# Performance work log

Hardware: AMD Instinct MI355X
Metric: run time of the kernel (lower is better)

Reference implementation:

```python
import jax, jax.numpy as jnp
import numpy as np

B, N, XD = 64, 512, 32  # batch, n_points, x_dims (feature columns); last 2 cols are t, y


def setup_inputs() -> dict:
    key = jax.random.key(0)
    xtys = jax.random.normal(key, (B, N, XD + 2), dtype=jnp.float32)
    return {"xtys": xtys}


def _linear_dml(xtys):
    b, n, D = xtys.shape
    d = D - 2
    xs = xtys[..., :d]          # (b, n, d) covariates
    ts = xtys[..., d]           # (b, n)   treatment
    ys = xtys[..., d + 1]       # (b, n)   outcome

    # Growing-prefix least squares via cumulative sufficient statistics.
    # For prefix i (rows 0..i): min-norm lstsq solution w = pinv(X^T X) X^T v == pinv(X) v,
    # matching torch.linalg.lstsq (gelsy/gelsd) semantics including rank-deficient prefixes.
    G = jnp.cumsum(jnp.einsum('bnd,bne->bnde', xs, xs), axis=1)      # (b,n,d,d) Gram
    Xty = jnp.cumsum(xs * ys[..., None], axis=1)                     # (b,n,d)
    Xtt = jnp.cumsum(xs * ts[..., None], axis=1)                     # (b,n,d)
    Sty = jnp.cumsum(ts * ys, axis=1)                                # (b,n)
    Stt = jnp.cumsum(ts * ts, axis=1)                                # (b,n)

    Ginv = jnp.linalg.pinv(G)                                        # batched pinv, (b,n,d,d)
    wy = jnp.einsum('bnde,bne->bnd', Ginv, Xty)
    wt = jnp.einsum('bnde,bne->bnd', Ginv, Xtt)

    # ate_i = <t_res, y_res> / <t_res, t_res> over prefix, expanded via the stats above.
    num = (Sty
           - jnp.einsum('bnd,bnd->bn', wt, Xty)
           - jnp.einsum('bnd,bnd->bn', wy, Xtt)
           + jnp.einsum('bnd,bnde,bne->bn', wt, G, wy))
    den = (Stt
           - 2.0 * jnp.einsum('bnd,bnd->bn', wt, Xtt)
           + jnp.einsum('bnd,bnde,bne->bn', wt, G, wt))
    safe = den > 0
    ate = jnp.where(safe, num / jnp.where(safe, den, 1.0), 0.0)      # min-norm: 0 when thats==0

    means = ate.at[:, 0].set(0.0)                                    # i==0 special case
    stds = jnp.zeros_like(means)                                     # module always appends zeros
    return means, 2.0 * jnp.log(stds)                                # -> -inf, as in the original


def reference(xtys):
    return _linear_dml(xtys)
```

## Files before the change

kernel.cpp:

```cpp
#include <hip/hip_runtime.h>
#include <math.h>
#include <utility>

#define BB 64
#define NN 512
#define DD 32
#define ZD 34
#define NE 595
#define WIN 8
#define NW 64
#define WACT 60

#define SEG 4
#define RS 128
#define KWS 16
#define CH 4
#define ECH 149
#define PSTRIDE 17

#define SPW 4

__device__ inline void ent2ij(int e, int& i, int& j) {
    int ii = 0, rem = e;
    while (rem >= ZD - ii) { rem -= (ZD - ii); ++ii; }
    i = ii; j = ii + rem;
}

template<int N> struct Pack { Pack<N - 1> head; float v; };
template<> struct Pack<1> { float v; };
template<int I, int N> __device__ __forceinline__ float& pget(Pack<N>& p) {
    static_assert(I < N, "oob");
    if constexpr (I == N - 1) return p.v;
    else return pget<I, N - 1>(p.head);
}

__device__ __forceinline__ float rdlane(float x, int srclane) {
    return __int_as_float(__builtin_amdgcn_readlane(__float_as_int(x), srclane));
}
__device__ __forceinline__ float bperm(int byteaddr, float x) {
    return __int_as_float(__builtin_amdgcn_ds_bpermute(byteaddr, __float_as_int(x)));
}

__global__ __launch_bounds__(256) void dml_gram(const float* __restrict__ xtys,
                                                float* __restrict__ P,
                                                float* __restrict__ out) {
    const int t   = threadIdx.x;
    const int blk = blockIdx.x;
    const int c   = blk % CH;
    const int bg  = blk / CH;
    const int g   = bg % SEG;
    const int b   = bg / SEG;

    const int gid = blk * 256 + t;
    if (gid < BB * NN) out[BB * NN + gid] = 0.0f;
    if (gid < BB * DD) out[(gid >> 5) * NN + (gid & 31)] = 0.0f;

    __shared__ float zs[RS * ZD];
    const float* src = xtys + ((size_t)b * NN + (size_t)g * RS) * ZD;
    for (int u = t; u < RS * ZD; u += 256) zs[u] = src[u];
    __syncthreads();

    const int e = c * ECH + t;
    if (t < ECH && e < NE) {
        int i, j;
        ent2ij(e, i, j);
        float* pdst = P + (size_t)(b * SEG + g) * PSTRIDE * NE + e;
        double acc = 0.0;
#pragma unroll
        for (int k = 0; k < KWS; ++k) {
            pdst[k * NE] = (float)acc;
#pragma unroll
            for (int s8 = 0; s8 < WIN; ++s8) {
                const float* row = &zs[(k * WIN + s8) * ZD];
                acc = fma((double)row[i], (double)row[j], acc);
            }
        }
        pdst[KWS * NE] = (float)acc;
    }
}


template<int R> __device__ __forceinline__
float initval(int j, int off_j, int zoff, const float* snL, const float* zb) {
    constexpr int RC = (R < DD) ? (R * ZD - (R * (R - 1)) / 2 - R) : 0;
    if constexpr (R < DD) {
        float v = 0.0f;
        if (j < DD) {
            int idx = (R < j) ? (RC + j) : (off_j + R);
            v = snL[idx];
        } else if (j < DD + WIN) {
            v = zb[zoff + R];
        } else if (j == 40) {
            v = snL[RC + DD];
        } else if (j == 41) {
            v = snL[RC + DD + 1];
        }
        return v;
    } else if constexpr (R < DD + WIN) {
        return (j < DD) ? zb[(R - DD) * ZD + j] : 0.0f;
    } else if constexpr (R == 40) {
        return (j < DD) ? snL[off_j + DD] : 0.0f;
    } else if constexpr (R == 41) {
        return (j < DD) ? snL[off_j + DD + 1] : 0.0f;
    } else {
        return 0.0f;
    }
}
template<int R> __device__ __forceinline__
void init_rec(Pack<48>& A, int j, int off_j, int zoff,
              const float* snL, const float* zb) {
    if constexpr (R < 48) {
        pget<R>(A) = initval<R>(j, off_j, zoff, snL, zb);
        init_rec<R + 1>(A, j, off_j, zoff, snL, zb);
    }
}

template<int K, int R> __device__ __forceinline__
void elim_rows(Pack<48>& A, float t) {
    if constexpr (R < DD + 10) {
        float fr = rdlane(pget<R>(A), K);
        pget<R>(A) = fmaf(-fr, t, pget<R>(A));
        elim_rows<K, R + 1>(A, t);
    }
}
template<int K> __device__ __forceinline__
void elim_step(Pack<48>& A) {
    float piv  = rdlane(pget<K>(A), K);
    float invp = (piv > 1e-30f) ? 1.0f / piv : 0.0f;
    float t    = invp * pget<K>(A);
    elim_rows<K, K + 1>(A, t);
}
template<int... Ks> __device__ __forceinline__
void elim_all(Pack<48>& A, std::integer_sequence<int, Ks...>) {
    ((elim_step<Ks>(A)), ...);
}

template<int R> __device__ __forceinline__
void kdump(Pack<48>& A, float* Kl, int c) {
    if constexpr (R < DD + 10) {
        Kl[(R - DD) * 10 + c] = -pget<R>(A);
        kdump<R + 1>(A, Kl, c);
    }
}

template<int L> __device__ __forceinline__
void tinit(Pack<12>& T, int row, int sys, const float* Kl, const float* zb) {
    if constexpr (L < 12) {
        float v;
        if constexpr (L < 8) {
            float kij = (row <= sys && L <= sys) ? Kl[row * 10 + L] : 0.0f;
            v = kij + ((row == L) ? 1.0f : 0.0f);
        } else if constexpr (L == 8)  v = (row <= sys) ? Kl[row * 10 + 8] : 0.0f;
        else if constexpr (L == 9)    v = (row <= sys) ? zb[row * ZD + DD] : 0.0f;
        else if constexpr (L == 10)   v = (row <= sys) ? Kl[row * 10 + 9] : 0.0f;
        else                          v = (row <= sys) ? zb[row * ZD + DD + 1] : 0.0f;
        pget<L>(T) = v;
        tinit<L + 1>(T, row, sys, Kl, zb);
    }
}
template<int K, int J> __device__ __forceinline__
void gjp_cols(Pack<12>& T, float f, int pb) {
    if constexpr (J < 12) {
        float pk = bperm(pb + 4 * K, pget<J>(T));
        pget<J>(T) = fmaf(-f, pk, pget<J>(T));
        gjp_cols<K, J + 1>(T, f, pb);
    }
}
template<int K> __device__ __forceinline__
void gjp_step(Pack<12>& T, int pb, int row, float& diag) {
    float pkK  = bperm(pb + 4 * K, pget<K>(T));
    float invp = (pkK > 1e-30f || pkK < -1e-30f) ? 1.0f / pkK : 0.0f;
    float f    = (row == K) ? 0.0f : pget<K>(T) * invp;
    gjp_cols<K, K + 1>(T, f, pb);
    if (row == K) diag = pget<K>(T);
}
template<int... Ks> __device__ __forceinline__
void gjp_all(Pack<12>& T, int pb, int row, float& diag,
             std::integer_sequence<int, Ks...>) {
    ((gjp_step<Ks>(T, pb, row, diag)), ...);
}

__global__ __launch_bounds__(256) void dml_solve(const float* __restrict__ xtys,
                                                 const float* __restrict__ P,
                                                 float* __restrict__ out) {
    const int wid  = threadIdx.x >> 6;
    const int lane = threadIdx.x & 63;
    const int id   = blockIdx.x * SPW + wid;
    const int w    = (id % WACT) + 4;
    const int b    = id / WACT;
    const int g    = w >> 4;
    const int k    = w & 15;

    __shared__ float snL[SPW][NE];
    __shared__ float zb[SPW][WIN * ZD];
    __shared__ float Kl[SPW][100];
    float* snW = snL[wid];
    float* zbW = zb[wid];
    float* KlW = Kl[wid];

    const float* pb_  = P + (size_t)b * SEG * PSTRIDE * NE;
    const float* src  = xtys + ((size_t)b * NN + (size_t)w * WIN) * ZD;
    for (int u = lane; u < NE; u += 64) {
        float v = pb_[(size_t)(g * PSTRIDE + k) * NE + u];
        for (int g2 = 0; g2 < g; ++g2)
            v += pb_[(size_t)(g2 * PSTRIDE + KWS) * NE + u];
        snW[u] = v;
    }
    for (int u = lane; u < WIN * ZD; u += 64) zbW[u] = src[u];

    const int j     = lane;
    const int off_j = j * (ZD - 1) - (j * (j - 1)) / 2;
    const int zoff  = (j - DD) * ZD;

    Pack<48> A;
    init_rec<0>(A, j, off_j, zoff, snW, zbW);

    elim_all(A, std::make_integer_sequence<int, DD>{});

    if (lane >= DD && lane < DD + 10) kdump<DD>(A, KlW, lane - DD);

    const int sys = lane >> 3;
    const int row = lane & 7;
    const int pb  = (threadIdx.x & ~7) << 2;

    Pack<12> T;
    tinit<0>(T, row, sys, KlW, zbW);
    float diag = 1.0f;
    gjp_all(T, pb, row, diag, std::make_integer_sequence<int, 8>{});

    float dinv = (diag > 1e-30f || diag < -1e-30f) ? 1.0f / diag : 0.0f;
    double s1 = (double)(pget<8>(T) * dinv);
    double s2 = (double)(pget<9>(T) * dinv);
    double r1 = (double)(pget<10>(T) * dinv);
    double r2 = (double)(pget<11>(T) * dinv);
    double gg = (double)KlW[80 + row] - (double)zbW[row * ZD + DD];
    double cd = gg * (s1 - s2);
    double cn = gg * (r1 - r2);
#pragma unroll
    for (int m = 1; m < 8; m <<= 1) {
        cd += __shfl_xor(cd, m, 8);
        cn += __shfl_xor(cn, m, 8);
    }

    double Stt0 = (double)snW[592];
    double Sty0 = (double)snW[593];
    double den  = Stt0 - (double)KlW[88] + cd;
    double num  = Sty0 - (double)KlW[89] + cn;
    double val  = (den > 0.0) ? num / den : 0.0;
    if (!isfinite(val)) val = 0.0;
    if (row == 0) out[b * NN + w * WIN + sys] = (float)val;
}

extern "C" void kernel_launch(void* const* d_in, const int* in_sizes, int n_in,
                              void* d_out, int out_size, void* d_ws, size_t ws_size,
                              hipStream_t stream) {
    const float* xtys = (const float*)d_in[0];
    float* out = (float*)d_out;
    float* P = (float*)d_ws;

    hipLaunchKernelGGL(dml_gram, dim3(BB * SEG * CH), dim3(256), 0, stream, xtys, P, out);
    hipLaunchKernelGGL(dml_solve, dim3(BB * WACT / SPW), dim3(256), 0, stream, xtys, P, out);
}
```

Baseline: 98.08 us.

## Pack three elimination systems per wavefront with two columns per lane

The solve kernel now runs one 64-lane block that handles three windows at once. For elimination, 21-lane groups each hold two matrix columns per lane (Pack<42> x2), and broadcasts use ds_bpermute instead of readlane. The 8x8 Gauss-Jordan stage then loops over the three windows in sequence. The aim is to cut idle lanes: the old layout left 22 of 64 lanes unused during elimination. The cost is roughly double the register use per lane, slower bpermute broadcasts in place of scalar readlane, and a serialized tail loop.

```diff
diff --git a/kernel.cpp b/kernel.cpp
--- a/kernel.cpp
+++ b/kernel.cpp
@@ -18,7 +18,7 @@
 #define ECH 149
 #define PSTRIDE 17
 
-#define SPW 4
+#define SPW3 3
 
 __device__ inline void ent2ij(int e, int& i, int& j) {
     int ii = 0, rem = e;
@@ -34,9 +34,6 @@
     else return pget<I, N - 1>(p.head);
 }
 
-__device__ __forceinline__ float rdlane(float x, int srclane) {
-    return __int_as_float(__builtin_amdgcn_readlane(__float_as_int(x), srclane));
-}
 __device__ __forceinline__ float bperm(int byteaddr, float x) {
     return __int_as_float(__builtin_amdgcn_ds_bpermute(byteaddr, __float_as_int(x)));
 }
@@ -81,65 +78,69 @@
 
 
 template<int R> __device__ __forceinline__
-float initval(int j, int off_j, int zoff, const float* snL, const float* zb) {
-    constexpr int RC = (R < DD) ? (R * ZD - (R * (R - 1)) / 2 - R) : 0;
-    if constexpr (R < DD) {
-        float v = 0.0f;
-        if (j < DD) {
-            int idx = (R < j) ? (RC + j) : (off_j + R);
-            v = snL[idx];
-        } else if (j < DD + WIN) {
-            v = zb[zoff + R];
-        } else if (j == 40) {
-            v = snL[RC + DD];
-        } else if (j == 41) {
-            v = snL[RC + DD + 1];
-        }
-        return v;
-    } else if constexpr (R < DD + WIN) {
-        return (j < DD) ? zb[(R - DD) * ZD + j] : 0.0f;
-    } else if constexpr (R == 40) {
-        return (j < DD) ? snL[off_j + DD] : 0.0f;
-    } else if constexpr (R == 41) {
-        return (j < DD) ? snL[off_j + DD + 1] : 0.0f;
-    } else {
-        return 0.0f;
-    }
-}
+void init2(Pack<42>& A0, Pack<42>& A1, int c0, int c1, int off0, int off1,
+           const float* snW, const float* zbW) {
+    if constexpr (R < 42) {
+        constexpr int CR = (R < DD) ? (R * ZD - (R * (R - 1)) / 2 - R) : 0;
+        float v0, v1;
+        if constexpr (R < DD) {
+            v0 = snW[(R < c0) ? (CR + c0) : (off0 + R)];
+            const float* p1;
+            if (c1 < DD)            p1 = &snW[(R < c1) ? (CR + c1) : (off1 + R)];
+            else if (c1 < DD + WIN) p1 = &zbW[(c1 - DD) * ZD + R];
+            else if (c1 == 40)      p1 = &snW[CR + DD];
+            else                    p1 = &snW[CR + DD + 1];
+            v1 = *p1;
+        } else if constexpr (R < DD + WIN) {
+            v0 = zbW[(R - DD) * ZD + c0];
+            v1 = (c1 < DD) ? zbW[(R - DD) * ZD + c1] : 0.0f;
+        } else if constexpr (R == 40) {
+            v0 = snW[off0 + DD];
+            v1 = (c1 < DD) ? snW[off1 + DD] : 0.0f;
+        } else {
+            v0 = snW[off0 + DD + 1];
+            v1 = (c1 < DD) ? snW[off1 + DD + 1] : 0.0f;
+        }
+        pget<R>(A0) = v0;
+        pget<R>(A1) = v1;
+        init2<R + 1>(A0, A1, c0, c1, off0, off1, snW, zbW);
+    }
+}
+
+template<int K, int R> __device__ __forceinline__
+void elim2_rows(Pack<42>& A0, Pack<42>& A1, float t0, float t1, int gb4) {
+    if constexpr (R < 42) {
+        float src;
+        if constexpr (K < 21) src = pget<R>(A0); else src = pget<R>(A1);
+        float fr = bperm(gb4 + 4 * (K < 21 ? K : K - 21), src);
+        if constexpr (K < 21)
+            pget<R>(A0) = fmaf(-fr, t0, pget<R>(A0));
+        pget<R>(A1) = fmaf(-fr, t1, pget<R>(A1));
+        elim2_rows<K, R + 1>(A0, A1, t0, t1, gb4);
+    }
+}
+template<int K> __device__ __forceinline__
+void elim2_step(Pack<42>& A0, Pack<42>& A1, int gb4) {
+    float srcK;
+    if constexpr (K < 21) srcK = pget<K>(A0); else srcK = pget<K>(A1);
+    float piv  = bperm(gb4 + 4 * (K < 21 ? K : K - 21), srcK);
+    float invp = (piv > 1e-30f) ? 1.0f / piv : 0.0f;
+    float t0   = invp * pget<K>(A0);
+    float t1   = invp * pget<K>(A1);
+    elim2_rows<K, K + 1>(A0, A1, t0, t1, gb4);
+}
+template<int... Ks> __device__ __forceinline__
+void elim2_all(Pack<42>& A0, Pack<42>& A1, int gb4,
+               std::integer_sequence<int, Ks...>) {
+    ((elim2_step<Ks>(A0, A1, gb4)), ...);
+}
+
 template<int R> __device__ __forceinline__
-void init_rec(Pack<48>& A, int j, int off_j, int zoff,
-              const float* snL, const float* zb) {
-    if constexpr (R < 48) {
-        pget<R>(A) = initval<R>(j, off_j, zoff, snL, zb);
-        init_rec<R + 1>(A, j, off_j, zoff, snL, zb);
-    }
-}
-
-template<int K, int R> __device__ __forceinline__
-void elim_rows(Pack<48>& A, float t) {
+void kdump2(Pack<42>& A1, float* Klg, int c10) {
     if constexpr (R < DD + 10) {
-        float fr = rdlane(pget<R>(A), K);
-        pget<R>(A) = fmaf(-fr, t, pget<R>(A));
-        elim_rows<K, R + 1>(A, t);
-    }
-}
-template<int K> __device__ __forceinline__
-void elim_step(Pack<48>& A) {
-    float piv  = rdlane(pget<K>(A), K);
-    float invp = (piv > 1e-30f) ? 1.0f / piv : 0.0f;
-    float t    = invp * pget<K>(A);
-    elim_rows<K, K + 1>(A, t);
-}
-template<int... Ks> __device__ __forceinline__
-void elim_all(Pack<48>& A, std::integer_sequence<int, Ks...>) {
-    ((elim_step<Ks>(A)), ...);
-}
-
-template<int R> __device__ __forceinline__
-void kdump(Pack<48>& A, float* Kl, int c) {
-    if constexpr (R < DD + 10) {
-        Kl[(R - DD) * 10 + c] = -pget<R>(A);
-        kdump<R + 1>(A, Kl, c);
+        if constexpr (R >= DD)
+            Klg[(R - DD) * 10 + c10] = -pget<R>(A1);
+        kdump2<R + 1>(A1, Klg, c10);
     }
 }
 
@@ -180,75 +181,90 @@
     ((gjp_step<Ks>(T, pb, row, diag)), ...);
 }
 
-__global__ __launch_bounds__(256) void dml_solve(const float* __restrict__ xtys,
-                                                 const float* __restrict__ P,
-                                                 float* __restrict__ out) {
-    const int wid  = threadIdx.x >> 6;
-    const int lane = threadIdx.x & 63;
-    const int id   = blockIdx.x * SPW + wid;
-    const int w    = (id % WACT) + 4;
-    const int b    = id / WACT;
-    const int g    = w >> 4;
-    const int k    = w & 15;
-
-    __shared__ float snL[SPW][NE];
-    __shared__ float zb[SPW][WIN * ZD];
-    __shared__ float Kl[SPW][100];
-    float* snW = snL[wid];
-    float* zbW = zb[wid];
-    float* KlW = Kl[wid];
-
-    const float* pb_  = P + (size_t)b * SEG * PSTRIDE * NE;
-    const float* src  = xtys + ((size_t)b * NN + (size_t)w * WIN) * ZD;
-    for (int u = lane; u < NE; u += 64) {
-        float v = pb_[(size_t)(g * PSTRIDE + k) * NE + u];
-        for (int g2 = 0; g2 < g; ++g2)
-            v += pb_[(size_t)(g2 * PSTRIDE + KWS) * NE + u];
-        snW[u] = v;
-    }
-    for (int u = lane; u < WIN * ZD; u += 64) zbW[u] = src[u];
-
-    const int j     = lane;
-    const int off_j = j * (ZD - 1) - (j * (j - 1)) / 2;
-    const int zoff  = (j - DD) * ZD;
-
-    Pack<48> A;
-    init_rec<0>(A, j, off_j, zoff, snW, zbW);
-
-    elim_all(A, std::make_integer_sequence<int, DD>{});
-
-    if (lane >= DD && lane < DD + 10) kdump<DD>(A, KlW, lane - DD);
+__global__ __launch_bounds__(64) void dml_solve(const float* __restrict__ xtys,
+                                                const float* __restrict__ P,
+                                                float* __restrict__ out) {
+    const int lane = threadIdx.x;
+    const int id0  = blockIdx.x * SPW3;
+
+    __shared__ float snS[SPW3 * NE];
+    __shared__ float zbS[SPW3 * WIN * ZD];
+    __shared__ float KlS[SPW3 * 100];
+
+    for (int q = 0; q < SPW3; ++q) {
+        const int idq = id0 + q;
+        const int w   = (idq % WACT) + 4;
+        const int b   = idq / WACT;
+        const int sg  = w >> 4;
+        const int kk  = w & 15;
+        const float* pb_ = P + (size_t)b * SEG * PSTRIDE * NE;
+        const float* src = xtys + ((size_t)b * NN + (size_t)w * WIN) * ZD;
+        float* snq = snS + q * NE;
+        float* zbq = zbS + q * (WIN * ZD);
+        for (int u = lane; u < NE; u += 64) {
+            float v = pb_[(size_t)(sg * PSTRIDE + kk) * NE + u];
+            for (int g2 = 0; g2 < sg; ++g2)
+                v += pb_[(size_t)(g2 * PSTRIDE + KWS) * NE + u];
+            snq[u] = v;
+        }
+        for (int u = lane; u < WIN * ZD; u += 64) zbq[u] = src[u];
+    }
+
+    const int g    = (lane >= 2 * 21) ? 2 : (lane / 21);
+    const int u    = lane - g * 21;
+    const int c0   = u;
+    const int c1   = u + 21;
+    const int off0 = c0 * (ZD - 1) - (c0 * (c0 - 1)) / 2;
+    const int off1 = c1 * (ZD - 1) - (c1 * (c1 - 1)) / 2;
+    const int gb4  = g * 21 * 4;
+    const float* snW = snS + g * NE;
+    const float* zbW = zbS + g * (WIN * ZD);
+
+    Pack<42> A0, A1;
+    init2<0>(A0, A1, c0, c1, off0, off1, snW, zbW);
+
+    elim2_all(A0, A1, gb4, std::make_integer_sequence<int, DD>{});
+
+    if (u >= 11 && u < 21) kdump2<0>(A1, (float*)(KlS + g * 100), u - 11);
 
     const int sys = lane >> 3;
     const int row = lane & 7;
-    const int pb  = (threadIdx.x & ~7) << 2;
-
-    Pack<12> T;
-    tinit<0>(T, row, sys, KlW, zbW);
-    float diag = 1.0f;
-    gjp_all(T, pb, row, diag, std::make_integer_sequence<int, 8>{});
-
-    float dinv = (diag > 1e-30f || diag < -1e-30f) ? 1.0f / diag : 0.0f;
-    double s1 = (double)(pget<8>(T) * dinv);
-    double s2 = (double)(pget<9>(T) * dinv);
-    double r1 = (double)(pget<10>(T) * dinv);
-    double r2 = (double)(pget<11>(T) * dinv);
-    double gg = (double)KlW[80 + row] - (double)zbW[row * ZD + DD];
-    double cd = gg * (s1 - s2);
-    double cn = gg * (r1 - r2);
+    const int pbB = (lane & ~7) << 2;
+
+    for (int q = 0; q < SPW3; ++q) {
+        const int idq = id0 + q;
+        const int w   = (idq % WACT) + 4;
+        const int b   = idq / WACT;
+        const float* Klq = KlS + q * 100;
+        const float* zbq = zbS + q * (WIN * ZD);
+
+        Pack<12> T;
+        tinit<0>(T, row, sys, Klq, zbq);
+        float diag = 1.0f;
+        gjp_all(T, pbB, row, diag, std::make_integer_sequence<int, 8>{});
+
+        float dinv = (diag > 1e-30f || diag < -1e-30f) ? 1.0f / diag : 0.0f;
+        double s1 = (double)(pget<8>(T) * dinv);
+        double s2 = (double)(pget<9>(T) * dinv);
+        double r1 = (double)(pget<10>(T) * dinv);
+        double r2 = (double)(pget<11>(T) * dinv);
+        double gg = (double)Klq[80 + row] - (double)zbq[row * ZD + DD];
+        double cd = gg * (s1 - s2);
+        double cn = gg * (r1 - r2);
 #pragma unroll
-    for (int m = 1; m < 8; m <<= 1) {
-        cd += __shfl_xor(cd, m, 8);
-        cn += __shfl_xor(cn, m, 8);
-    }
-
-    double Stt0 = (double)snW[592];
-    double Sty0 = (double)snW[593];
-    double den  = Stt0 - (double)KlW[88] + cd;
-    double num  = Sty0 - (double)KlW[89] + cn;
-    double val  = (den > 0.0) ? num / den : 0.0;
-    if (!isfinite(val)) val = 0.0;
-    if (row == 0) out[b * NN + w * WIN + sys] = (float)val;
+        for (int m = 1; m < 8; m <<= 1) {
+            cd += __shfl_xor(cd, m, 8);
+            cn += __shfl_xor(cn, m, 8);
+        }
+
+        double Stt0 = (double)snS[q * NE + 592];
+        double Sty0 = (double)snS[q * NE + 593];
+        double den  = Stt0 - (double)Klq[88] + cd;
+        double num  = Sty0 - (double)Klq[89] + cn;
+        double val  = (den > 0.0) ? num / den : 0.0;
+        if (!isfinite(val)) val = 0.0;
+        if (row == 0) out[b * NN + w * WIN + sys] = (float)val;
+    }
 }
 
 extern "C" void kernel_launch(void* const* d_in, const int* in_sizes, int n_in,
@@ -259,5 +275,5 @@
     float* P = (float*)d_ws;
 
     hipLaunchKernelGGL(dml_gram, dim3(BB * SEG * CH), dim3(256), 0, stream, xtys, P, out);
-    hipLaunchKernelGGL(dml_solve, dim3(BB * WACT / SPW), dim3(256), 0, stream, xtys, P, out);
-}
+    hipLaunchKernelGGL(dml_solve, dim3(BB * WACT / SPW3), dim3(64), 0, stream, xtys, P, out);
+}
```

Result: slower. 109.5 us (+11.7%).
